# Optimization experiments

Hardware: AMD Instinct MI355X
Metric: run time of the kernel (lower is better)

## Reference

```python
import jax, jax.numpy as jnp
import numpy as np

B, N_WAY, N_SHOT, QUERY, NUM_SLOT, D = 64, 5, 5, 15, 8, 640
LAMBDA = 0.1
NEG_INF = jnp.float32(-1e30)


def cover_select(scores):
    # scores: [b, n_way, num_slot]. For each class in order, greedily pick the
    # highest-scoring slot not already taken (replicates torch sort+dedup loop).
    def per_batch(s):
        def step(taken, row):
            sel = jnp.argmax(jnp.where(taken, NEG_INF, row))
            return taken.at[sel].set(True), sel
        _, sel = jax.lax.scan(step, jnp.zeros(s.shape[-1], dtype=bool), s)
        return sel  # [n_way]
    return jax.vmap(per_batch)(scores)  # [b, n_way]


def euclid(gallery, query):
    # gallery [b, n, d], query [b, m, d] -> [b, m, n]
    return jnp.sum((query[:, :, None, :] - gallery[:, None, :, :]) ** 2, axis=-1)


def loss_acc(proto, q, labels_query):
    diff = euclid(proto, q)                                   # [b, n_way*query, n_way]
    logits = jax.nn.log_softmax(-diff, axis=2)
    logits = logits.reshape(B, QUERY, N_WAY, N_WAY)
    nll = -jnp.take_along_axis(logits, labels_query, axis=3).mean()
    y_hat = jnp.argmax(logits, axis=3)
    acc = (y_hat == labels_query[..., 0]).astype(jnp.float32).mean()
    return nll, acc


def setup_inputs() -> dict:
    key = jax.random.key(0)
    k0, k1, k2, k3 = jax.random.split(key, 4)
    n_total = B * N_WAY * (N_SHOT + QUERY)
    out_f = jax.random.normal(k0, (n_total, NUM_SLOT, D), dtype=jnp.float32)
    labels_support = jax.random.randint(k1, (B, N_SHOT, N_WAY, 1), 0, N_WAY, dtype=jnp.int32)
    labels_query = jax.random.randint(k2, (B, QUERY, N_WAY, 1), 0, N_WAY, dtype=jnp.int32)
    att_loss = jax.random.uniform(k3, (1,), dtype=jnp.float32)
    return {"out_f": out_f, "labels_support": labels_support,
            "labels_query": labels_query, "att_loss": att_loss}


def reference(out_f, labels_support, labels_query, att_loss):
    # mode == 'train' path of SimilarityLoss.forward
    b, d = B, out_f.shape[-1]
    ns = b * N_WAY * N_SHOT
    # class prototypes over shots: [b*n_way, num_slot, d]
    sup = out_f[:ns].reshape(b * N_WAY, N_SHOT, NUM_SLOT, d).mean(1)
    qry = out_f[ns:].reshape(b, N_WAY, QUERY, NUM_SLOT, d)

    max_s = cover_select(sup.mean(-1).reshape(b, N_WAY, NUM_SLOT))  # [b, n_way]

    sup_b = sup.reshape(b, N_WAY, NUM_SLOT, d)
    # proto[j, c] = sup_b[j, c, max_s[j, c]]
    proto = jax.vmap(jax.vmap(lambda s, i: s[i]))(sup_b, max_s)     # [b, n_way, d]

    # get_selected path: each class's queries pick that class's selected slot
    out_query = jax.vmap(jax.vmap(lambda q, i: q[:, i, :]))(qry, max_s)  # [b, n_way, query, d]
    out_query = out_query.reshape(b, N_WAY * QUERY, d)

    # get_22 path (faithful to the original non-reset record_temp accumulation):
    # for image s, pick among rows {q22[j, s', max_s[j, i]] : s' <= s, i < n_way}
    # the row with the largest mean over d.
    imgs = N_WAY * QUERY
    q22 = qry.reshape(b, imgs, NUM_SLOT, d)
    cand = jax.vmap(lambda q, i: q[:, i, :])(q22, max_s)            # [b, imgs, n_way, d]
    L = imgs * N_WAY
    m = cand.mean(-1).reshape(b, L)                                 # flat order (s, i)
    prefix = jnp.arange(L)[None, :] < ((jnp.arange(imgs) + 1) * N_WAY)[:, None]  # [imgs, L]
    k = jnp.argmax(jnp.where(prefix[None], m[:, None, :], NEG_INF), axis=-1)     # [b, imgs]
    out_query_t = jnp.take_along_axis(cand.reshape(b, L, d), k[:, :, None], axis=1)  # [b, imgs, d]

    nll, acc = loss_acc(proto, out_query, labels_query)
    loss = nll + jnp.float32(LAMBDA) * att_loss[0]
    loss_t, acc_t = loss_acc(proto, out_query_t, labels_query)
    return (loss, loss_t, acc, acc_t)
```

## Files before the change

kernel.cpp:

```cpp
#include <hip/hip_runtime.h>

#define BB 64
#define N_WAY 5
#define N_SHOT 5
#define QUERY 15
#define NUM_SLOT 8
#define DD 640
#define IMGS (N_WAY * QUERY)
#define NS (BB * N_WAY * N_SHOT)
#define NROWS 6400
#define ROWSZ (NUM_SLOT * DD)
#define F4_PER_SLOT 160
#define NELEM (BB * IMGS)
#define NGROUP (BB * N_WAY)
#define NTASK 150
#define TPB 8
#define SBLK 19
#define LBLK 19

__global__ __launch_bounds__(256) void k_pass1(const float* __restrict__ out_f,
                                               float* __restrict__ rowmean,
                                               float* __restrict__ proto_all,
                                               float* __restrict__ pn2_all) {
    int b = blockIdx.x;
    int t = threadIdx.x;
    int slot = t >> 5;
    int l = t & 31;
    if (b < NGROUP) {
        const int g = b;
        float4 acc[5];
        #pragma unroll
        for (int k = 0; k < 5; ++k) acc[k] = make_float4(0.f, 0.f, 0.f, 0.f);
        #pragma unroll
        for (int sh = 0; sh < N_SHOT; ++sh) {
            const float4* p = (const float4*)(out_f +
                ((size_t)((g * N_SHOT + sh) * NUM_SLOT + slot)) * DD);
            float s = 0.f;
            #pragma unroll
            for (int k = 0; k < 5; ++k) {
                float4 v = p[l + k * 32];
                acc[k].x += v.x; acc[k].y += v.y; acc[k].z += v.z; acc[k].w += v.w;
                s += (v.x + v.y) + (v.z + v.w);
            }
            #pragma unroll
            for (int off = 16; off; off >>= 1) s += __shfl_down(s, off, 32);
            if (l == 0) rowmean[(g * N_SHOT + sh) * NUM_SLOT + slot] = s * (1.f / DD);
        }
        float4* pp = (float4*)(proto_all + ((size_t)(g * NUM_SLOT + slot)) * DD);
        float ssq = 0.f;
        #pragma unroll
        for (int k = 0; k < 5; ++k) {
            acc[k].x *= 0.2f; acc[k].y *= 0.2f; acc[k].z *= 0.2f; acc[k].w *= 0.2f;
            pp[l + k * 32] = acc[k];
            ssq += acc[k].x * acc[k].x + acc[k].y * acc[k].y
                 + acc[k].z * acc[k].z + acc[k].w * acc[k].w;
        }
        #pragma unroll
        for (int off = 16; off; off >>= 1) ssq += __shfl_down(ssq, off, 32);
        if (l == 0) pn2_all[g * NUM_SLOT + slot] = ssq;
    } else {
        int r = NS + (b - NGROUP);
        const float4* p = (const float4*)(out_f + (size_t)r * ROWSZ) + slot * F4_PER_SLOT;
        float s = 0.f;
        #pragma unroll
        for (int k = 0; k < 5; ++k) {
            float4 v = p[l + k * 32];
            s += (v.x + v.y) + (v.z + v.w);
        }
        #pragma unroll
        for (int off = 16; off; off >>= 1) s += __shfl_down(s, off, 32);
        if (l == 0) rowmean[r * NUM_SLOT + slot] = s * (1.f / DD);
    }
}

__global__ __launch_bounds__(64) void k_select(const float* __restrict__ rowmean,
                                               const float* __restrict__ pn2_all,
                                               int* __restrict__ max_s,
                                               int* __restrict__ k_idx,
                                               float* __restrict__ p2c) {
    int j = blockIdx.x;
    int t = threadIdx.x;
    __shared__ float supm[N_WAY * NUM_SLOT];
    __shared__ int msS[N_WAY];
    __shared__ float qb[IMGS * NUM_SLOT];

    const float* qbase = rowmean + (size_t)(NS + j * IMGS) * NUM_SLOT;
    for (int i = t; i < IMGS * NUM_SLOT; i += 64) qb[i] = qbase[i];
    if (t < N_WAY * NUM_SLOT) {
        int c = t >> 3, s = t & 7;
        const float* sb = rowmean + (size_t)j * (N_WAY * N_SHOT * NUM_SLOT)
                          + c * (N_SHOT * NUM_SLOT) + s;
        float a = sb[0] + sb[8] + sb[16] + sb[24] + sb[32];
        supm[t] = a * 0.2f;
    }
    __syncthreads();

    if (t == 0) {
        unsigned taken = 0u;
        #pragma unroll
        for (int c = 0; c < N_WAY; ++c) {
            float best = -3.0e38f; int bi = 0;
            #pragma unroll
            for (int s = 0; s < NUM_SLOT; ++s) {
                float v = supm[c * NUM_SLOT + s];
                if (!((taken >> s) & 1u) && v > best) { best = v; bi = s; }
            }
            taken |= (1u << bi);
            msS[c] = bi;
            max_s[j * N_WAY + c] = bi;
        }
    }
    __syncthreads();
    int ms0 = msS[0], ms1 = msS[1], ms2 = msS[2], ms3 = msS[3], ms4 = msS[4];

    if (t < N_WAY) p2c[j * N_WAY + t] = pn2_all[(j * N_WAY + t) * NUM_SLOT + msS[t]];

    float bv; int bi;
    {
        const float* q = &qb[t * NUM_SLOT];
        bv = q[ms0]; bi = t * N_WAY;
        float v;
        v = q[ms1]; if (v > bv) { bv = v; bi = t * N_WAY + 1; }
        v = q[ms2]; if (v > bv) { bv = v; bi = t * N_WAY + 2; }
        v = q[ms3]; if (v > bv) { bv = v; bi = t * N_WAY + 3; }
        v = q[ms4]; if (v > bv) { bv = v; bi = t * N_WAY + 4; }
    }
    #pragma unroll
    for (int off = 1; off < 64; off <<= 1) {
        float ov = __shfl_up(bv, off, 64);
        int   oi = __shfl_up(bi, off, 64);
        if (t >= off && !(bv > ov)) { bv = ov; bi = oi; }
    }
    k_idx[j * IMGS + t] = bi;
    float tv = __shfl(bv, 63, 64);
    int   ti = __shfl(bi, 63, 64);
    float bv2 = -3.0e38f; int bi2 = 0;
    if (t < IMGS - 64) {
        int s = 64 + t;
        const float* q = &qb[s * NUM_SLOT];
        bv2 = q[ms0]; bi2 = s * N_WAY;
        float v;
        v = q[ms1]; if (v > bv2) { bv2 = v; bi2 = s * N_WAY + 1; }
        v = q[ms2]; if (v > bv2) { bv2 = v; bi2 = s * N_WAY + 2; }
        v = q[ms3]; if (v > bv2) { bv2 = v; bi2 = s * N_WAY + 3; }
        v = q[ms4]; if (v > bv2) { bv2 = v; bi2 = s * N_WAY + 4; }
    }
    #pragma unroll
    for (int off = 1; off < 16; off <<= 1) {
        float ov = __shfl_up(bv2, off, 64);
        int   oi = __shfl_up(bi2, off, 64);
        if (t >= off && t < IMGS - 64 && !(bv2 > ov)) { bv2 = ov; bi2 = oi; }
    }
    if (t < IMGS - 64) {
        if (!(bv2 > tv)) { bv2 = tv; bi2 = ti; }
        k_idx[j * IMGS + 64 + t] = bi2;
    }
}

__global__ __launch_bounds__(256) void k_score(const float* __restrict__ out_f,
                                               const float* __restrict__ proto_all,
                                               const int* __restrict__ max_s,
                                               const int* __restrict__ k_idx,
                                               float* __restrict__ score) {
    int blk = blockIdx.x;
    int j = blk / SBLK, bt = blk - j * SBLK;
    int t = threadIdx.x;
    int wave = t >> 6, lane = t & 63;

    __shared__ __align__(16) float protoS[N_WAY * DD];
    __shared__ int msS[N_WAY];

    if (t < N_WAY) msS[t] = max_s[j * N_WAY + t];
    __syncthreads();
    for (int i = t; i < N_WAY * F4_PER_SLOT; i += 256) {
        int c = i / F4_PER_SLOT, r = i - c * F4_PER_SLOT;
        ((float4*)protoS)[i] = ((const float4*)(proto_all +
            ((size_t)((j * N_WAY + c) * NUM_SLOT + msS[c])) * DD))[r];
    }
    __syncthreads();

    #pragma unroll
    for (int rnd = 0; rnd < 2; ++rnd) {
        int task = bt * TPB + rnd * 4 + wave;
        if (task >= NTASK) continue;
        int row, sl;
        if (task < IMGS) {
            row = task;
            sl = msS[task / QUERY];
        } else {
            int m = task - IMGS;
            int kk = k_idx[j * IMGS + m];
            int s2 = kk / N_WAY, c2 = kk - s2 * N_WAY;
            row = s2;
            sl = msS[c2];
        }
        const float2* q = (const float2*)(out_f +
            (size_t)(NS + j * IMGS + row) * ROWSZ + sl * DD) + lane * 5;
        float2 qv[5];
        #pragma unroll
        for (int k = 0; k < 5; ++k) qv[k] = q[k];
        float acc[N_WAY] = {0, 0, 0, 0, 0};
        #pragma unroll
        for (int n = 0; n < N_WAY; ++n) {
            const float2* pp = (const float2*)(protoS + n * DD) + lane * 5;
            #pragma unroll
            for (int k = 0; k < 5; ++k) {
                float2 pv = pp[k];
                acc[n] += qv[k].x * pv.x + qv[k].y * pv.y;
            }
        }
        #pragma unroll
        for (int n = 0; n < N_WAY; ++n) {
            #pragma unroll
            for (int off = 32; off; off >>= 1)
                acc[n] += __shfl_down(acc[n], off, 64);
        }
        if (lane == 0) {
            float* dst = score + ((size_t)j * NTASK + task) * N_WAY;
            #pragma unroll
            for (int n = 0; n < N_WAY; ++n) dst[n] = acc[n];
        }
    }
}

__global__ __launch_bounds__(256) void k_loss2(const float* __restrict__ score,
                                               const float* __restrict__ p2c,
                                               const int* __restrict__ labels_query,
                                               float4* __restrict__ part) {
    int t = threadIdx.x;
    int e = blockIdx.x * 256 + t;
    float nll1 = 0.f, nll2 = 0.f, acc1 = 0.f, acc2 = 0.f;
    if (e < NELEM) {
        int j = e / IMGS, m = e - j * IMGS;
        int label = labels_query[e];
        const float* p2 = p2c + j * N_WAY;
        const float* sc1 = score + ((size_t)j * NTASK + m) * N_WAY;
        const float* sc2 = score + ((size_t)j * NTASK + IMGS + m) * N_WAY;
        {
            float li[N_WAY]; float mx = -3.0e38f;
            #pragma unroll
            for (int n = 0; n < N_WAY; ++n) { li[n] = 2.f * sc1[n] - p2[n]; mx = fmaxf(mx, li[n]); }
            float se = 0.f;
            #pragma unroll
            for (int n = 0; n < N_WAY; ++n) se += expf(li[n] - mx);
            float lse = mx + logf(se);
            int bi = 0; float bv = li[0];
            #pragma unroll
            for (int n = 1; n < N_WAY; ++n) if (li[n] > bv) { bv = li[n]; bi = n; }
            nll1 = -(li[label] - lse);
            acc1 = (bi == label) ? 1.f : 0.f;
        }
        {
            float li[N_WAY]; float mx = -3.0e38f;
            #pragma unroll
            for (int n = 0; n < N_WAY; ++n) { li[n] = 2.f * sc2[n] - p2[n]; mx = fmaxf(mx, li[n]); }
            float se = 0.f;
            #pragma unroll
            for (int n = 0; n < N_WAY; ++n) se += expf(li[n] - mx);
            float lse = mx + logf(se);
            int bi = 0; float bv = li[0];
            #pragma unroll
            for (int n = 1; n < N_WAY; ++n) if (li[n] > bv) { bv = li[n]; bi = n; }
            nll2 = -(li[label] - lse);
            acc2 = (bi == label) ? 1.f : 0.f;
        }
    }
    __shared__ float4 red[256];
    red[t] = make_float4(nll1, nll2, acc1, acc2);
    __syncthreads();
    for (int w = 128; w; w >>= 1) {
        if (t < w) {
            red[t].x += red[t + w].x; red[t].y += red[t + w].y;
            red[t].z += red[t + w].z; red[t].w += red[t + w].w;
        }
        __syncthreads();
    }
    if (t == 0) part[blockIdx.x] = red[0];
}

__global__ __launch_bounds__(64) void k_final(const float4* __restrict__ part,
                                              const float* __restrict__ att_loss,
                                              float* __restrict__ out) {
    int t = threadIdx.x;
    float4 v = (t < LBLK) ? part[t] : make_float4(0.f, 0.f, 0.f, 0.f);
    #pragma unroll
    for (int off = 32; off; off >>= 1) {
        v.x += __shfl_down(v.x, off, 64);
        v.y += __shfl_down(v.y, off, 64);
        v.z += __shfl_down(v.z, off, 64);
        v.w += __shfl_down(v.w, off, 64);
    }
    if (t == 0) {
        out[0] = v.x / (float)NELEM + 0.1f * att_loss[0];
        out[1] = v.y / (float)NELEM;
        out[2] = v.z / (float)NELEM;
        out[3] = v.w / (float)NELEM;
    }
}

extern "C" void kernel_launch(void* const* d_in, const int* in_sizes, int n_in,
                              void* d_out, int out_size, void* d_ws, size_t ws_size,
                              hipStream_t stream) {
    const float* out_f        = (const float*)d_in[0];
    const int*   labels_query = (const int*)d_in[2];
    const float* att_loss     = (const float*)d_in[3];
    float* out = (float*)d_out;

    float*  rowmean   = (float*)d_ws;
    float*  proto_all = rowmean + NROWS * NUM_SLOT;
    float*  pn2_all   = proto_all + NGROUP * NUM_SLOT * DD;
    float*  score     = pn2_all + NGROUP * NUM_SLOT;
    float*  p2c       = score + (size_t)BB * NTASK * N_WAY;
    float4* part      = (float4*)(p2c + NGROUP);
    int*    max_s     = (int*)(part + LBLK);
    int*    k_idx     = max_s + NGROUP;

    k_pass1<<<NGROUP + NELEM, 256, 0, stream>>>(out_f, rowmean, proto_all, pn2_all);
    k_select<<<BB, 64, 0, stream>>>(rowmean, pn2_all, max_s, k_idx, p2c);
    k_score<<<BB * SBLK, 256, 0, stream>>>(out_f, proto_all, max_s, k_idx, score);
    k_loss2<<<LBLK, 256, 0, stream>>>(score, p2c, labels_query, part);
    k_final<<<1, 64, 0, stream>>>(part, att_loss, out);
}
```

Measured before the change: 45.47 us.

## Fuse select, score and loss kernels into one per-batch block kernel

Merges k_select, k_score and k_loss2 into a single kernel with one 512-thread block per batch. Selected slots, k indices and scores stay in shared memory instead of going through global memory, and prototypes are held in registers. This removes two launches and the global round trips between them. The cost is that the scoring stage drops from 1216 blocks to 64, so far fewer CUs share the query-row gathers.

New measurement: 49.45 us. 1.09x slower.

```diff
diff --git a/kernel.cpp b/kernel.cpp
--- a/kernel.cpp
+++ b/kernel.cpp
@@ -14,9 +14,6 @@
 #define NELEM (BB * IMGS)
 #define NGROUP (BB * N_WAY)
 #define NTASK 150
-#define TPB 8
-#define SBLK 19
-#define LBLK 19
 
 __global__ __launch_bounds__(256) void k_pass1(const float* __restrict__ out_f,
                                                float* __restrict__ rowmean,
@@ -73,25 +70,32 @@
     }
 }
 
-__global__ __launch_bounds__(64) void k_select(const float* __restrict__ rowmean,
-                                               const float* __restrict__ pn2_all,
-                                               int* __restrict__ max_s,
-                                               int* __restrict__ k_idx,
-                                               float* __restrict__ p2c) {
+__global__ __launch_bounds__(512) void k_mega(const float* __restrict__ out_f,
+                                              const float* __restrict__ rowmean,
+                                              const float* __restrict__ proto_all,
+                                              const float* __restrict__ pn2_all,
+                                              const int* __restrict__ labels_query,
+                                              float4* __restrict__ part) {
     int j = blockIdx.x;
     int t = threadIdx.x;
+    int wave = t >> 6, lane = t & 63;
+
+    __shared__ __align__(16) float qb[IMGS * NUM_SLOT];
     __shared__ float supm[N_WAY * NUM_SLOT];
-    __shared__ int msS[N_WAY];
-    __shared__ float qb[IMGS * NUM_SLOT];
+    __shared__ int   msS[N_WAY];
+    __shared__ float p2S[N_WAY];
+    __shared__ int   kS[IMGS];
+    __shared__ float scS[NTASK * N_WAY];
+    __shared__ float4 redS[128];
 
     const float* qbase = rowmean + (size_t)(NS + j * IMGS) * NUM_SLOT;
-    for (int i = t; i < IMGS * NUM_SLOT; i += 64) qb[i] = qbase[i];
-    if (t < N_WAY * NUM_SLOT) {
-        int c = t >> 3, s = t & 7;
+    if (t < 150) ((float4*)qb)[t] = ((const float4*)qbase)[t];
+    if (t >= 256 && t < 256 + N_WAY * NUM_SLOT) {
+        int idx = t - 256;
+        int c = idx >> 3, s = idx & 7;
         const float* sb = rowmean + (size_t)j * (N_WAY * N_SHOT * NUM_SLOT)
                           + c * (N_SHOT * NUM_SLOT) + s;
-        float a = sb[0] + sb[8] + sb[16] + sb[24] + sb[32];
-        supm[t] = a * 0.2f;
+        supm[idx] = (sb[0] + sb[8] + sb[16] + sb[24] + sb[32]) * 0.2f;
     }
     __syncthreads();
 
@@ -107,139 +111,118 @@
             }
             taken |= (1u << bi);
             msS[c] = bi;
-            max_s[j * N_WAY + c] = bi;
-        }
-    }
-    __syncthreads();
-    int ms0 = msS[0], ms1 = msS[1], ms2 = msS[2], ms3 = msS[3], ms4 = msS[4];
-
-    if (t < N_WAY) p2c[j * N_WAY + t] = pn2_all[(j * N_WAY + t) * NUM_SLOT + msS[t]];
-
-    float bv; int bi;
-    {
-        const float* q = &qb[t * NUM_SLOT];
-        bv = q[ms0]; bi = t * N_WAY;
-        float v;
-        v = q[ms1]; if (v > bv) { bv = v; bi = t * N_WAY + 1; }
-        v = q[ms2]; if (v > bv) { bv = v; bi = t * N_WAY + 2; }
-        v = q[ms3]; if (v > bv) { bv = v; bi = t * N_WAY + 3; }
-        v = q[ms4]; if (v > bv) { bv = v; bi = t * N_WAY + 4; }
-    }
+        }
+    }
+    __syncthreads();
+
+    if (t >= 448 && t < 448 + N_WAY) {
+        int n = t - 448;
+        p2S[n] = pn2_all[(j * N_WAY + n) * NUM_SLOT + msS[n]];
+    }
+
+    float2 pv[N_WAY][5];
     #pragma unroll
-    for (int off = 1; off < 64; off <<= 1) {
-        float ov = __shfl_up(bv, off, 64);
-        int   oi = __shfl_up(bi, off, 64);
-        if (t >= off && !(bv > ov)) { bv = ov; bi = oi; }
-    }
-    k_idx[j * IMGS + t] = bi;
-    float tv = __shfl(bv, 63, 64);
-    int   ti = __shfl(bi, 63, 64);
-    float bv2 = -3.0e38f; int bi2 = 0;
-    if (t < IMGS - 64) {
-        int s = 64 + t;
-        const float* q = &qb[s * NUM_SLOT];
-        bv2 = q[ms0]; bi2 = s * N_WAY;
-        float v;
-        v = q[ms1]; if (v > bv2) { bv2 = v; bi2 = s * N_WAY + 1; }
-        v = q[ms2]; if (v > bv2) { bv2 = v; bi2 = s * N_WAY + 2; }
-        v = q[ms3]; if (v > bv2) { bv2 = v; bi2 = s * N_WAY + 3; }
-        v = q[ms4]; if (v > bv2) { bv2 = v; bi2 = s * N_WAY + 4; }
-    }
-    #pragma unroll
-    for (int off = 1; off < 16; off <<= 1) {
-        float ov = __shfl_up(bv2, off, 64);
-        int   oi = __shfl_up(bi2, off, 64);
-        if (t >= off && t < IMGS - 64 && !(bv2 > ov)) { bv2 = ov; bi2 = oi; }
-    }
-    if (t < IMGS - 64) {
-        if (!(bv2 > tv)) { bv2 = tv; bi2 = ti; }
-        k_idx[j * IMGS + 64 + t] = bi2;
-    }
-}
-
-__global__ __launch_bounds__(256) void k_score(const float* __restrict__ out_f,
-                                               const float* __restrict__ proto_all,
-                                               const int* __restrict__ max_s,
-                                               const int* __restrict__ k_idx,
-                                               float* __restrict__ score) {
-    int blk = blockIdx.x;
-    int j = blk / SBLK, bt = blk - j * SBLK;
-    int t = threadIdx.x;
-    int wave = t >> 6, lane = t & 63;
-
-    __shared__ __align__(16) float protoS[N_WAY * DD];
-    __shared__ int msS[N_WAY];
-
-    if (t < N_WAY) msS[t] = max_s[j * N_WAY + t];
-    __syncthreads();
-    for (int i = t; i < N_WAY * F4_PER_SLOT; i += 256) {
-        int c = i / F4_PER_SLOT, r = i - c * F4_PER_SLOT;
-        ((float4*)protoS)[i] = ((const float4*)(proto_all +
-            ((size_t)((j * N_WAY + c) * NUM_SLOT + msS[c])) * DD))[r];
-    }
-    __syncthreads();
-
-    #pragma unroll
-    for (int rnd = 0; rnd < 2; ++rnd) {
-        int task = bt * TPB + rnd * 4 + wave;
-        if (task >= NTASK) continue;
-        int row, sl;
-        if (task < IMGS) {
-            row = task;
-            sl = msS[task / QUERY];
-        } else {
-            int m = task - IMGS;
-            int kk = k_idx[j * IMGS + m];
-            int s2 = kk / N_WAY, c2 = kk - s2 * N_WAY;
-            row = s2;
-            sl = msS[c2];
-        }
-        const float2* q = (const float2*)(out_f +
-            (size_t)(NS + j * IMGS + row) * ROWSZ + sl * DD) + lane * 5;
-        float2 qv[5];
-        #pragma unroll
-        for (int k = 0; k < 5; ++k) qv[k] = q[k];
-        float acc[N_WAY] = {0, 0, 0, 0, 0};
-        #pragma unroll
-        for (int n = 0; n < N_WAY; ++n) {
-            const float2* pp = (const float2*)(protoS + n * DD) + lane * 5;
-            #pragma unroll
-            for (int k = 0; k < 5; ++k) {
-                float2 pv = pp[k];
-                acc[n] += qv[k].x * pv.x + qv[k].y * pv.y;
-            }
-        }
-        #pragma unroll
-        for (int n = 0; n < N_WAY; ++n) {
-            #pragma unroll
-            for (int off = 32; off; off >>= 1)
-                acc[n] += __shfl_down(acc[n], off, 64);
-        }
-        if (lane == 0) {
-            float* dst = score + ((size_t)j * NTASK + task) * N_WAY;
-            #pragma unroll
-            for (int n = 0; n < N_WAY; ++n) dst[n] = acc[n];
-        }
-    }
-}
-
-__global__ __launch_bounds__(256) void k_loss2(const float* __restrict__ score,
-                                               const float* __restrict__ p2c,
-                                               const int* __restrict__ labels_query,
-                                               float4* __restrict__ part) {
-    int t = threadIdx.x;
-    int e = blockIdx.x * 256 + t;
-    float nll1 = 0.f, nll2 = 0.f, acc1 = 0.f, acc2 = 0.f;
-    if (e < NELEM) {
-        int j = e / IMGS, m = e - j * IMGS;
-        int label = labels_query[e];
-        const float* p2 = p2c + j * N_WAY;
-        const float* sc1 = score + ((size_t)j * NTASK + m) * N_WAY;
-        const float* sc2 = score + ((size_t)j * NTASK + IMGS + m) * N_WAY;
+    for (int n = 0; n < N_WAY; ++n) {
+        const float2* pp = (const float2*)(proto_all +
+            ((size_t)((j * N_WAY + n) * NUM_SLOT + msS[n])) * DD) + lane * 5;
+        #pragma unroll
+        for (int k = 0; k < 5; ++k) pv[n][k] = pp[k];
+    }
+
+    if (wave == 0) {
+        int ms0 = msS[0], ms1 = msS[1], ms2 = msS[2], ms3 = msS[3], ms4 = msS[4];
+        float bv; int bi;
+        {
+            const float* q = &qb[lane * NUM_SLOT];
+            bv = q[ms0]; bi = lane * N_WAY;
+            float v;
+            v = q[ms1]; if (v > bv) { bv = v; bi = lane * N_WAY + 1; }
+            v = q[ms2]; if (v > bv) { bv = v; bi = lane * N_WAY + 2; }
+            v = q[ms3]; if (v > bv) { bv = v; bi = lane * N_WAY + 3; }
+            v = q[ms4]; if (v > bv) { bv = v; bi = lane * N_WAY + 4; }
+        }
+        #pragma unroll
+        for (int off = 1; off < 64; off <<= 1) {
+            float ov = __shfl_up(bv, off, 64);
+            int   oi = __shfl_up(bi, off, 64);
+            if (lane >= off && !(bv > ov)) { bv = ov; bi = oi; }
+        }
+        kS[lane] = bi;
+        float tv = __shfl(bv, 63, 64);
+        int   ti = __shfl(bi, 63, 64);
+        float bv2 = -3.0e38f; int bi2 = 0;
+        if (lane < IMGS - 64) {
+            int s = 64 + lane;
+            const float* q = &qb[s * NUM_SLOT];
+            bv2 = q[ms0]; bi2 = s * N_WAY;
+            float v;
+            v = q[ms1]; if (v > bv2) { bv2 = v; bi2 = s * N_WAY + 1; }
+            v = q[ms2]; if (v > bv2) { bv2 = v; bi2 = s * N_WAY + 2; }
+            v = q[ms3]; if (v > bv2) { bv2 = v; bi2 = s * N_WAY + 3; }
+            v = q[ms4]; if (v > bv2) { bv2 = v; bi2 = s * N_WAY + 4; }
+        }
+        #pragma unroll
+        for (int off = 1; off < 16; off <<= 1) {
+            float ov = __shfl_up(bv2, off, 64);
+            int   oi = __shfl_up(bi2, off, 64);
+            if (lane >= off && lane < IMGS - 64 && !(bv2 > ov)) { bv2 = ov; bi2 = oi; }
+        }
+        if (lane < IMGS - 64) {
+            if (!(bv2 > tv)) { bv2 = tv; bi2 = ti; }
+            kS[64 + lane] = bi2;
+        }
+    }
+    __syncthreads();
+
+    for (int r = 0; r < 19; ++r) {
+        int task = r * 8 + wave;
+        if (task < NTASK) {
+            int row, sl;
+            if (task < IMGS) {
+                row = task;
+                sl = msS[task / QUERY];
+            } else {
+                int m = task - IMGS;
+                int kk = kS[m];
+                int s2 = kk / N_WAY, c2 = kk - s2 * N_WAY;
+                row = s2;
+                sl = msS[c2];
+            }
+            const float2* q = (const float2*)(out_f +
+                (size_t)(NS + j * IMGS + row) * ROWSZ + sl * DD) + lane * 5;
+            float2 qv[5];
+            #pragma unroll
+            for (int k = 0; k < 5; ++k) qv[k] = q[k];
+            float acc[N_WAY] = {0, 0, 0, 0, 0};
+            #pragma unroll
+            for (int n = 0; n < N_WAY; ++n) {
+                #pragma unroll
+                for (int k = 0; k < 5; ++k)
+                    acc[n] += qv[k].x * pv[n][k].x + qv[k].y * pv[n][k].y;
+            }
+            #pragma unroll
+            for (int n = 0; n < N_WAY; ++n) {
+                #pragma unroll
+                for (int off = 32; off; off >>= 1)
+                    acc[n] += __shfl_down(acc[n], off, 64);
+            }
+            if (lane == 0) {
+                #pragma unroll
+                for (int n = 0; n < N_WAY; ++n) scS[task * N_WAY + n] = acc[n];
+            }
+        }
+    }
+    __syncthreads();
+
+    float4 lv = make_float4(0.f, 0.f, 0.f, 0.f);
+    if (t < IMGS) {
+        int label = labels_query[j * IMGS + t];
+        const float* sc1 = &scS[t * N_WAY];
+        const float* sc2 = &scS[(IMGS + t) * N_WAY];
         {
             float li[N_WAY]; float mx = -3.0e38f;
             #pragma unroll
-            for (int n = 0; n < N_WAY; ++n) { li[n] = 2.f * sc1[n] - p2[n]; mx = fmaxf(mx, li[n]); }
+            for (int n = 0; n < N_WAY; ++n) { li[n] = 2.f * sc1[n] - p2S[n]; mx = fmaxf(mx, li[n]); }
             float se = 0.f;
             #pragma unroll
             for (int n = 0; n < N_WAY; ++n) se += expf(li[n] - mx);
@@ -247,13 +230,13 @@
             int bi = 0; float bv = li[0];
             #pragma unroll
             for (int n = 1; n < N_WAY; ++n) if (li[n] > bv) { bv = li[n]; bi = n; }
-            nll1 = -(li[label] - lse);
-            acc1 = (bi == label) ? 1.f : 0.f;
+            lv.x = -(li[label] - lse);
+            lv.z = (bi == label) ? 1.f : 0.f;
         }
         {
             float li[N_WAY]; float mx = -3.0e38f;
             #pragma unroll
-            for (int n = 0; n < N_WAY; ++n) { li[n] = 2.f * sc2[n] - p2[n]; mx = fmaxf(mx, li[n]); }
+            for (int n = 0; n < N_WAY; ++n) { li[n] = 2.f * sc2[n] - p2S[n]; mx = fmaxf(mx, li[n]); }
             float se = 0.f;
             #pragma unroll
             for (int n = 0; n < N_WAY; ++n) se += expf(li[n] - mx);
@@ -261,28 +244,27 @@
             int bi = 0; float bv = li[0];
             #pragma unroll
             for (int n = 1; n < N_WAY; ++n) if (li[n] > bv) { bv = li[n]; bi = n; }
-            nll2 = -(li[label] - lse);
-            acc2 = (bi == label) ? 1.f : 0.f;
-        }
-    }
-    __shared__ float4 red[256];
-    red[t] = make_float4(nll1, nll2, acc1, acc2);
-    __syncthreads();
-    for (int w = 128; w; w >>= 1) {
+            lv.y = -(li[label] - lse);
+            lv.w = (bi == label) ? 1.f : 0.f;
+        }
+    }
+    if (t < 128) redS[t] = lv;
+    __syncthreads();
+    for (int w = 64; w; w >>= 1) {
         if (t < w) {
-            red[t].x += red[t + w].x; red[t].y += red[t + w].y;
-            red[t].z += red[t + w].z; red[t].w += red[t + w].w;
+            redS[t].x += redS[t + w].x; redS[t].y += redS[t + w].y;
+            redS[t].z += redS[t + w].z; redS[t].w += redS[t + w].w;
         }
         __syncthreads();
     }
-    if (t == 0) part[blockIdx.x] = red[0];
+    if (t == 0) part[j] = redS[0];
 }
 
 __global__ __launch_bounds__(64) void k_final(const float4* __restrict__ part,
                                               const float* __restrict__ att_loss,
                                               float* __restrict__ out) {
     int t = threadIdx.x;
-    float4 v = (t < LBLK) ? part[t] : make_float4(0.f, 0.f, 0.f, 0.f);
+    float4 v = part[t];
     #pragma unroll
     for (int off = 32; off; off >>= 1) {
         v.x += __shfl_down(v.x, off, 64);
@@ -309,15 +291,10 @@
     float*  rowmean   = (float*)d_ws;
     float*  proto_all = rowmean + NROWS * NUM_SLOT;
     float*  pn2_all   = proto_all + NGROUP * NUM_SLOT * DD;
-    float*  score     = pn2_all + NGROUP * NUM_SLOT;
-    float*  p2c       = score + (size_t)BB * NTASK * N_WAY;
-    float4* part      = (float4*)(p2c + NGROUP);
-    int*    max_s     = (int*)(part + LBLK);
-    int*    k_idx     = max_s + NGROUP;
+    float4* part      = (float4*)(pn2_all + NGROUP * NUM_SLOT);
 
     k_pass1<<<NGROUP + NELEM, 256, 0, stream>>>(out_f, rowmean, proto_all, pn2_all);
-    k_select<<<BB, 64, 0, stream>>>(rowmean, pn2_all, max_s, k_idx, p2c);
-    k_score<<<BB * SBLK, 256, 0, stream>>>(out_f, proto_all, max_s, k_idx, score);
-    k_loss2<<<LBLK, 256, 0, stream>>>(score, p2c, labels_query, part);
+    k_mega<<<BB, 512, 0, stream>>>(out_f, rowmean, proto_all, pn2_all,
+                                   labels_query, part);
     k_final<<<1, 64, 0, stream>>>(part, att_loss, out);
 }
```
